# Kernel optimization log

Measured on AMD Instinct MI355X. Metric: run time of the kernel, lower is better.

Reference implementation:

```python
import jax, jax.numpy as jnp
import numpy as np

T, B, I, H, O = 1024, 256, 256, 256, 256


def setup_inputs() -> dict:
    key = jax.random.key(0)
    ks = jax.random.split(key, 12)
    s = 0.01  # init scale matching np.random.normal(0, 0.01)
    return {
        "x_steps": jax.random.normal(ks[0], (T, B, I), dtype=jnp.float32),
        "h": jnp.zeros((B, H), dtype=jnp.float32),
        "w_xr": s * jax.random.normal(ks[1], (I, H), dtype=jnp.float32),
        "w_hr": s * jax.random.normal(ks[2], (H, H), dtype=jnp.float32),
        "b_r": jnp.zeros((H,), dtype=jnp.float32),
        "w_xz": s * jax.random.normal(ks[3], (I, H), dtype=jnp.float32),
        "w_hz": s * jax.random.normal(ks[4], (H, H), dtype=jnp.float32),
        "b_z": jnp.zeros((H,), dtype=jnp.float32),
        "w_xh": s * jax.random.normal(ks[5], (I, H), dtype=jnp.float32),
        "w_hh": s * jax.random.normal(ks[6], (H, H), dtype=jnp.float32),
        "b_h": jnp.zeros((H,), dtype=jnp.float32),
        "w_out": s * jax.random.normal(ks[7], (H, O), dtype=jnp.float32),
        "b_out": jnp.zeros((O,), dtype=jnp.float32),
    }


def reference(x_steps, h, w_xr, w_hr, b_r, w_xz, w_hz, b_z,
              w_xh, w_hh, b_h, w_out, b_out):
    # Precompute all input projections in one batched GEMM per gate: [T,B,H]
    xr = jnp.einsum('tbi,ih->tbh', x_steps, w_xr) + b_r
    xz = jnp.einsum('tbi,ih->tbh', x_steps, w_xz) + b_z
    xh = jnp.einsum('tbi,ih->tbh', x_steps, w_xh) + b_h

    def step(h, xs):
        xr_t, xz_t, xh_t = xs
        r = jax.nn.sigmoid(xr_t + h @ w_hr)
        z = jax.nn.sigmoid(xz_t + h @ w_hz)
        cand = jnp.tanh(xh_t + (r * h) @ w_hh)
        h_new = h * z + (1.0 - z) * cand
        # NOTE: original emits matmul(cand, W_out)+b, using the candidate,
        # not the updated hidden state -- replicate faithfully.
        out = cand @ w_out + b_out
        return h_new, out

    h_final, outs = jax.lax.scan(step, h, (xr, xz, xh))  # outs: [T,B,O]
    return outs.reshape(T * B, O), h_final  # torch.cat(result_list, dim=0)
```

## Files before the change

### kernel.cpp

```cpp
#include <hip/hip_runtime.h>


typedef unsigned short u16t;
typedef unsigned int   u32t;
typedef unsigned long long u64t;
typedef short  s16x8 __attribute__((ext_vector_type(8)));
typedef float  f32x4 __attribute__((ext_vector_type(4)));
typedef float  f32v4 __attribute__((ext_vector_type(4)));
typedef u32t   u32x2 __attribute__((ext_vector_type(2)));

#define L2E 1.4426950408889634f
#define NCONS 112

#define BAR_LDS() asm volatile("s_waitcnt lgkmcnt(0)\n\ts_barrier" ::: "memory")
#define PIN(v) asm volatile("" : "+v"(v))

__device__ __forceinline__ float lo_f(u32t u) {
  return __builtin_bit_cast(float, u << 16);
}
__device__ __forceinline__ float hi_f(u32t u) {
  return __builtin_bit_cast(float, u & 0xffff0000u);
}
__device__ __forceinline__ u32t f2bf(float f) {
  u32t u = __builtin_bit_cast(u32t, f);
  return (u + 0x7fffu + ((u >> 16) & 1u)) >> 16;
}
__device__ __forceinline__ u32t cvtpk(float lo, float hi) {
  u32t r;
  asm("v_cvt_pk_bf16_f32 %0, %1, %2" : "=v"(r) : "v"(lo), "v"(hi));
  return r;
}
__device__ __forceinline__ f32x4 MF(s16x8 a, s16x8 b, f32x4 c) {
  return __builtin_amdgcn_mfma_f32_16x16x32_bf16(a, b, c, 0, 0, 0);
}
__device__ __forceinline__ float sigm2(float y) {
  return __builtin_amdgcn_rcpf(1.0f + __builtin_amdgcn_exp2f(-y));
}
__device__ __forceinline__ float tanh2(float y) {
  return fmaf(-2.0f, __builtin_amdgcn_rcpf(__builtin_amdgcn_exp2f(y) + 1.0f), 1.0f);
}

__global__ void pack_w(const float* __restrict__ wxr, const float* __restrict__ wxz,
                       const float* __restrict__ wxh, const float* __restrict__ whr,
                       const float* __restrict__ whz, const float* __restrict__ whh,
                       const float* __restrict__ wout, u16t* __restrict__ dst,
                       int* __restrict__ prog) {
  if (blockIdx.x == 0 && threadIdx.x < 16) prog[threadIdx.x] = 0;
  int e = blockIdx.x * 256 + threadIdx.x;
  int mat = e >> 16, i = e & 65535;
  const float* src = mat == 0 ? wxr : mat == 1 ? wxz : mat == 2 ? wxh
                   : mat == 3 ? whr : mat == 4 ? whz : mat == 5 ? whh : wout;
  float sc = (mat == 2 || mat == 5) ? 2.0f * L2E : (mat == 6 ? 1.0f : L2E);
  int j = i & 7, lane = (i >> 3) & 63, ks = (i >> 9) & 7, nb = i >> 12;
  int k = ks * 32 + (lane >> 4) * 8 + j;
  int n = nb * 16 + (lane & 15);
  dst[e] = (u16t)f2bf(src[k * 256 + n] * sc);
}

__global__ __launch_bounds__(512, 2) void gru_xproj(
    const float* __restrict__ x, const u16t* __restrict__ wpack,
    const float* __restrict__ br, const float* __restrict__ bz,
    const float* __restrict__ bh,
    u16t* __restrict__ xr_p, u16t* __restrict__ xz_p, u16t* __restrict__ xh_p) {
  __shared__ __align__(128) u16t xt[16384];
  const int tid = threadIdx.x, bid = blockIdx.x;
  const int t = bid >> 2, b0 = (bid & 3) * 64;
  const float* xrow = x + ((size_t)t * 256 + b0) * 256;
#pragma unroll
  for (int c = 0; c < 8; ++c) {
    int f4 = c * 512 + tid;
    f32v4 v = ((const f32v4*)xrow)[f4];
    u32t lo = f2bf(v[0]) | (f2bf(v[1]) << 16);
    u32t hi = f2bf(v[2]) | (f2bf(v[3]) << 16);
    int row = f4 >> 6, c8 = (f4 & 63) * 8;
    int off = (row * 512 + c8) ^ ((row & 7) << 4);
    u32x2 vv; vv[0] = lo; vv[1] = hi;
    *(u32x2*)((char*)xt + off) = vv;
  }
  __syncthreads();
  const int lane = tid & 63, w = tid >> 6;
  const int m2 = w & 1, cg = w >> 1;
  const int arow = m2 * 32 + (lane & 15);
  const int abase = arow * 512 + (lane >> 4) * 16;
  const int asw = (lane & 7) << 4;
  const f32x4 Z = {0.f, 0.f, 0.f, 0.f};
  f32x4 acc[2][12];
#pragma unroll
  for (int s = 0; s < 2; ++s)
#pragma unroll
    for (int p = 0; p < 12; ++p) acc[s][p] = Z;
#pragma unroll
  for (int ks = 0; ks < 8; ++ks) {
    s16x8 a0 = *(const s16x8*)((char*)xt + ((abase + ks * 64) ^ asw));
    s16x8 a1 = *(const s16x8*)((char*)xt + ((abase + 16 * 512 + ks * 64) ^ asw));
#pragma unroll
    for (int p = 0; p < 12; ++p) {
      int pj = cg * 12 + p;
      int gate = pj >> 4, nb = pj & 15;
      const s16x8* wb = (const s16x8*)wpack + gate * 8192;
      s16x8 b = wb[(nb * 8 + ks) * 64 + lane];
      acc[0][p] = MF(a0, b, acc[0][p]);
      acc[1][p] = MF(a1, b, acc[1][p]);
    }
  }
#pragma unroll
  for (int p = 0; p < 12; ++p) {
    int pj = cg * 12 + p;
    int gate = pj >> 4, nb = pj & 15;
    const float* bp = gate == 0 ? br : gate == 1 ? bz : bh;
    float bs = (gate == 2) ? 2.0f * L2E : L2E;
    float bv = bp[nb * 16 + (lane & 15)] * bs;
    u16t* op = gate == 0 ? xr_p : gate == 1 ? xz_p : xh_p;
#pragma unroll
    for (int s = 0; s < 2; ++s) {
      int wg = (b0 >> 4) + m2 * 2 + s;
      u32t lo = f2bf(acc[s][p][0] + bv) | (f2bf(acc[s][p][1] + bv) << 16);
      u32t hi = f2bf(acc[s][p][2] + bv) | (f2bf(acc[s][p][3] + bv) << 16);
      size_t off = (gate == 2)
          ? (size_t)t * 16384 + wg * 1024 + nb * 64 + lane
          : (size_t)t * 32768 + wg * 1024 + nb * 64 + lane;
      u32x2 vv; vv[0] = lo; vv[1] = hi;
      ((u32x2*)op)[off] = vv;
    }
  }
}

#define OFFSW(row, colx2) (((row) * 512 + (colx2)) ^ (((row) & 7) << 4))
#define LDA_HB(ks) (*(const s16x8*)((char*)hb + ((aoff + (ks) * 64) ^ asw)))
#define LDA_RH(ks) (*(const s16x8*)((char*)rh + ((aoff + (ks) * 64) ^ asw)))
#define ZLOAD(buf, ks) do { buf[0] = pz[(ks) * 64]; buf[1] = pz[(ks) * 64 + 512]; } while (0)
#define G1_STEP(buf, ks) do { s16x8 a_ = LDA_HB(ks); \
    ar0 = MF(a_, whr_r[0][ks], ar0); ar1 = MF(a_, whr_r[1][ks], ar1); \
    az0 = MF(a_, buf[0], az0);       az1 = MF(a_, buf[1], az1); } while (0)

__global__ __launch_bounds__(512, 2) void gru_fused(
    const float* __restrict__ h0, const u16t* __restrict__ wpack,
    const u16t* __restrict__ xr_p, const u16t* __restrict__ xz_p,
    const u16t* __restrict__ xh_p, u16t* __restrict__ cand_w,
    const u16t* __restrict__ cand_r, float* __restrict__ hout,
    int* __restrict__ prog, const float* __restrict__ bout,
    float* __restrict__ out) {
  __shared__ __align__(128) u16t smem[16384];
  const int tid = threadIdx.x, lane = tid & 63, w = tid >> 6;
  const int bid = blockIdx.x;

  if (bid < 16) {
    u16t* hb = smem;
    u16t* rh = smem + 4096;
    const int wg = bid;
    const int rlo = (lane >> 4) * 4;
    const int cA = w * 32 + (lane & 15);

    float hr_[2][4];
#pragma unroll
    for (int c = 0; c < 2; ++c)
#pragma unroll
      for (int j = 0; j < 4; ++j)
        hr_[c][j] = h0[(size_t)(wg * 16 + rlo + j) * 256 + cA + c * 16];
#pragma unroll
    for (int c = 0; c < 2; ++c)
#pragma unroll
      for (int j = 0; j < 4; ++j)
        *(u16t*)((char*)hb + OFFSW(rlo + j, (cA + c * 16) * 2)) = (u16t)f2bf(hr_[c][j]);
    __syncthreads();

    const s16x8* pz = (const s16x8*)wpack + 4 * 8192 + w * 1024 + lane;
    const int aoff = (lane & 15) * 512 + (lane >> 4) * 16;
    const int asw = (lane & 7) << 4;

    s16x8 whr_r[2][8], whh_r[2][8];
    {
      const s16x8* prw = (const s16x8*)wpack + 3 * 8192;
      const s16x8* phw = (const s16x8*)wpack + 5 * 8192;
#pragma unroll
      for (int c = 0; c < 2; ++c)
#pragma unroll
        for (int ks = 0; ks < 8; ++ks) {
          int fo = ((2 * w + c) * 8 + ks) * 64 + lane;
          whr_r[c][ks] = prw[fo]; PIN(whr_r[c][ks]);
          whh_r[c][ks] = phw[fo]; PIN(whh_r[c][ks]);
        }
    }

    const size_t xoffRZ = (size_t)wg * 1024 + w * 128 + lane;
    const size_t xoffH  = (size_t)wg * 1024 + w * 128 + lane;
    const u32x2* PXR = (const u32x2*)xr_p;
    const u32x2* PXZ = (const u32x2*)xz_p;
    const u32x2* PXH = (const u32x2*)xh_p;
    u32x2* SXH = (u32x2*)cand_w;

    u32x2 vxr0 = PXR[xoffRZ], vxr1 = PXR[xoffRZ + 64];
    u32x2 vxz0 = PXZ[xoffRZ], vxz1 = PXZ[xoffRZ + 64];
    u32x2 vxh0 = PXH[xoffH],  vxh1 = PXH[xoffH + 64];

    s16x8 bA[2], bB[2];
    ZLOAD(bA, 0);
    ZLOAD(bB, 1);

    for (int t = 0; t < 1024; ++t) {
      f32x4 ar0, ar1, az0, az1;
      ar0[0] = lo_f(vxr0[0]); ar0[1] = hi_f(vxr0[0]); ar0[2] = lo_f(vxr0[1]); ar0[3] = hi_f(vxr0[1]);
      ar1[0] = lo_f(vxr1[0]); ar1[1] = hi_f(vxr1[0]); ar1[2] = lo_f(vxr1[1]); ar1[3] = hi_f(vxr1[1]);
      az0[0] = lo_f(vxz0[0]); az0[1] = hi_f(vxz0[0]); az0[2] = lo_f(vxz0[1]); az0[3] = hi_f(vxz0[1]);
      az1[0] = lo_f(vxz1[0]); az1[1] = hi_f(vxz1[0]); az1[2] = lo_f(vxz1[1]); az1[3] = hi_f(vxz1[1]);

      G1_STEP(bA, 0); ZLOAD(bA, 2);
      G1_STEP(bB, 1); ZLOAD(bB, 3);
      G1_STEP(bA, 2); ZLOAD(bA, 4);
      G1_STEP(bB, 3); ZLOAD(bB, 5);
      G1_STEP(bA, 4); ZLOAD(bA, 6);
      G1_STEP(bB, 5); ZLOAD(bB, 7);
      G1_STEP(bA, 6);
      G1_STEP(bB, 7);

      float r_[2][4];
      r_[0][0] = sigm2(ar0[0]); r_[0][1] = sigm2(ar0[1]); r_[0][2] = sigm2(ar0[2]); r_[0][3] = sigm2(ar0[3]);
      r_[1][0] = sigm2(ar1[0]); r_[1][1] = sigm2(ar1[1]); r_[1][2] = sigm2(ar1[2]); r_[1][3] = sigm2(ar1[3]);

#pragma unroll
      for (int c = 0; c < 2; ++c) {
        u32t p01 = cvtpk(r_[c][0] * hr_[c][0], r_[c][1] * hr_[c][1]);
        u32t p23 = cvtpk(r_[c][2] * hr_[c][2], r_[c][3] * hr_[c][3]);
        *(u16t*)((char*)rh + OFFSW(rlo + 0, (cA + c * 16) * 2)) = (u16t)p01;
        *(u16t*)((char*)rh + OFFSW(rlo + 1, (cA + c * 16) * 2)) = (u16t)(p01 >> 16);
        *(u16t*)((char*)rh + OFFSW(rlo + 2, (cA + c * 16) * 2)) = (u16t)p23;
        *(u16t*)((char*)rh + OFFSW(rlo + 3, (cA + c * 16) * 2)) = (u16t)(p23 >> 16);
      }
      BAR_LDS();

      float z_[2][4];
      z_[0][0] = sigm2(az0[0]); z_[0][1] = sigm2(az0[1]); z_[0][2] = sigm2(az0[2]); z_[0][3] = sigm2(az0[3]);
      z_[1][0] = sigm2(az1[0]); z_[1][1] = sigm2(az1[1]); z_[1][2] = sigm2(az1[2]); z_[1][3] = sigm2(az1[3]);

      f32x4 ac0, ac1;
      ac0[0] = lo_f(vxh0[0]); ac0[1] = hi_f(vxh0[0]); ac0[2] = lo_f(vxh0[1]); ac0[3] = hi_f(vxh0[1]);
      ac1[0] = lo_f(vxh1[0]); ac1[1] = hi_f(vxh1[0]); ac1[2] = lo_f(vxh1[1]); ac1[3] = hi_f(vxh1[1]);

      {
        int tn = t < 1023 ? t + 1 : t;
        size_t oRZ = xoffRZ + (size_t)tn * 32768;
        size_t oH  = xoffH + (size_t)tn * 16384;
        vxr0 = PXR[oRZ]; vxr1 = PXR[oRZ + 64];
        vxz0 = PXZ[oRZ]; vxz1 = PXZ[oRZ + 64];
        vxh0 = PXH[oH];  vxh1 = PXH[oH + 64];
      }

#pragma unroll
      for (int ks = 0; ks < 8; ++ks) {
        s16x8 a_ = LDA_RH(ks);
        ac0 = MF(a_, whh_r[0][ks], ac0);
        ac1 = MF(a_, whh_r[1][ks], ac1);
      }

      float cd[2][4];
      cd[0][0] = tanh2(ac0[0]); cd[0][1] = tanh2(ac0[1]); cd[0][2] = tanh2(ac0[2]); cd[0][3] = tanh2(ac0[3]);
      cd[1][0] = tanh2(ac1[0]); cd[1][1] = tanh2(ac1[1]); cd[1][2] = tanh2(ac1[2]); cd[1][3] = tanh2(ac1[3]);

      size_t ocur = xoffH + (size_t)t * 16384;
      u32x2 s0, s1;
      s0[0] = cvtpk(cd[0][0], cd[0][1]); s0[1] = cvtpk(cd[0][2], cd[0][3]);
      s1[0] = cvtpk(cd[1][0], cd[1][1]); s1[1] = cvtpk(cd[1][2], cd[1][3]);
      __hip_atomic_store((u64t*)(SXH + ocur), __builtin_bit_cast(u64t, s0),
                         __ATOMIC_RELAXED, __HIP_MEMORY_SCOPE_AGENT);
      __hip_atomic_store((u64t*)(SXH + ocur + 64), __builtin_bit_cast(u64t, s1),
                         __ATOMIC_RELAXED, __HIP_MEMORY_SCOPE_AGENT);

#pragma unroll
      for (int c = 0; c < 2; ++c) {
#pragma unroll
        for (int j = 0; j < 4; ++j)
          hr_[c][j] = fmaf(z_[c][j], hr_[c][j] - cd[c][j], cd[c][j]);
        u32t p01 = cvtpk(hr_[c][0], hr_[c][1]);
        u32t p23 = cvtpk(hr_[c][2], hr_[c][3]);
        *(u16t*)((char*)hb + OFFSW(rlo + 0, (cA + c * 16) * 2)) = (u16t)p01;
        *(u16t*)((char*)hb + OFFSW(rlo + 1, (cA + c * 16) * 2)) = (u16t)(p01 >> 16);
        *(u16t*)((char*)hb + OFFSW(rlo + 2, (cA + c * 16) * 2)) = (u16t)p23;
        *(u16t*)((char*)hb + OFFSW(rlo + 3, (cA + c * 16) * 2)) = (u16t)(p23 >> 16);
      }

      ZLOAD(bA, 0);
      ZLOAD(bB, 1);
      BAR_LDS();

      if ((t & 15) == 15) {
        __syncthreads();
        if (tid == 0)
          __hip_atomic_store(prog + wg, t + 1, __ATOMIC_RELAXED,
                             __HIP_MEMORY_SCOPE_AGENT);
      }
    }
#pragma unroll
    for (int c = 0; c < 2; ++c)
#pragma unroll
      for (int j = 0; j < 4; ++j)
        hout[(size_t)(wg * 16 + rlo + j) * 256 + cA + c * 16] = hr_[c][j];

  } else {
    u16t* cm = smem;
    const int cid = bid - 16;
    const s16x8* wo = (const s16x8*)wpack + 6 * 8192;
    const int mt = w & 3, nbs = (w >> 2) * 8;
    const int arow = mt * 16 + (lane & 15);
    const int abase = arow * 512 + (lane >> 4) * 16;
    const int asw = (lane & 7) << 4;
    const f32x4 Z = {0.f, 0.f, 0.f, 0.f};
    int lastmn = 0;

    for (int tile = cid; tile < 4096; tile += NCONS) {
      const int t = tile >> 2, q = tile & 3;
      const int need = t + 1;
      if (lastmn < need) {
        if (tid == 0) {
          int mn;
          for (;;) {
            mn = 1 << 30;
#pragma unroll
            for (int s = 0; s < 16; ++s)
              mn = min(mn, __hip_atomic_load(prog + s, __ATOMIC_RELAXED,
                                             __HIP_MEMORY_SCOPE_AGENT));
            if (mn >= need) break;
            __builtin_amdgcn_s_sleep(8);
            __builtin_amdgcn_s_sleep(8);
            __builtin_amdgcn_s_sleep(8);
            __builtin_amdgcn_s_sleep(8);
          }
          *(int*)cm = mn;
        }
        __syncthreads();
        lastmn = *(volatile int*)cm;
        __syncthreads();
      }
      const u32x2* src = (const u32x2*)cand_r + ((size_t)t * 16 + q * 4) * 1024;
#pragma unroll
      for (int it = 0; it < 8; ++it) {
        int i = it * 512 + tid;
        u32x2 v = __builtin_nontemporal_load(src + i);
        int wg_l = i >> 10, nb = (i >> 6) & 15, ls = i & 63;
        int brow = wg_l * 16 + (ls >> 4) * 4;
        int hc2 = (nb * 16 + (ls & 15)) * 2;
        u16t ev[4] = {(u16t)(v[0] & 0xffff), (u16t)(v[0] >> 16),
                      (u16t)(v[1] & 0xffff), (u16t)(v[1] >> 16)};
#pragma unroll
        for (int j = 0; j < 4; ++j)
          *(u16t*)((char*)cm + OFFSW(brow + j, hc2)) = ev[j];
      }
      __syncthreads();
      f32x4 acc[8] = {Z, Z, Z, Z, Z, Z, Z, Z};
#pragma unroll
      for (int ks = 0; ks < 8; ++ks) {
        s16x8 a = *(const s16x8*)((char*)cm + ((abase + ks * 64) ^ asw));
#pragma unroll
        for (int p = 0; p < 8; ++p)
          acc[p] = MF(a, wo[((nbs + p) * 8 + ks) * 64 + lane], acc[p]);
      }
#pragma unroll
      for (int p = 0; p < 8; ++p) {
        int col = (nbs + p) * 16 + (lane & 15);
        float bv = bout[col];
        size_t rb = (size_t)t * 256 + q * 64 + mt * 16 + (lane >> 4) * 4;
#pragma unroll
        for (int j = 0; j < 4; ++j)
          __builtin_nontemporal_store(acc[p][j] + bv, &out[(rb + j) * 256 + col]);
      }
      __syncthreads();
    }
  }
}

extern "C" void kernel_launch(void* const* d_in, const int* in_sizes, int n_in,
                              void* d_out, int out_size, void* d_ws, size_t ws_size,
                              hipStream_t stream) {
  const float* x    = (const float*)d_in[0];
  const float* h0   = (const float*)d_in[1];
  const float* wxr  = (const float*)d_in[2];
  const float* whr  = (const float*)d_in[3];
  const float* br   = (const float*)d_in[4];
  const float* wxz  = (const float*)d_in[5];
  const float* whz  = (const float*)d_in[6];
  const float* bz   = (const float*)d_in[7];
  const float* wxh  = (const float*)d_in[8];
  const float* whh  = (const float*)d_in[9];
  const float* bh   = (const float*)d_in[10];
  const float* wout = (const float*)d_in[11];
  const float* bout = (const float*)d_in[12];

  float* out  = (float*)d_out;
  u16t* wpack = (u16t*)d_ws;
  int*  prog  = (int*)((char*)d_ws + 917504);
  u16t* xh_p  = (u16t*)((char*)d_ws + (1u << 20));
  u16t* xr_p  = (u16t*)d_out;
  u16t* xz_p  = (u16t*)d_out + 65536;
  float* hout = (float*)((char*)d_out + 268435456ull);

  pack_w<<<1792, 256, 0, stream>>>(wxr, wxz, wxh, whr, whz, whh, wout, wpack, prog);
  gru_xproj<<<4096, 512, 0, stream>>>(x, wpack, br, bz, bh, xr_p, xz_p, xh_p);
  gru_fused<<<16 + NCONS, 512, 0, stream>>>(h0, wpack, xr_p, xz_p, xh_p,
                                            xh_p, xh_p, hout, prog, bout, out);
}
```

Measured before the change: 2.441 ms.

## Fuse input projection into persistent kernel, overlapping it with the recurrence

```diff
diff --git a/kernel.cpp b/kernel.cpp
--- a/kernel.cpp
+++ b/kernel.cpp
@@ -39,13 +39,22 @@
 __device__ __forceinline__ float tanh2(float y) {
   return fmaf(-2.0f, __builtin_amdgcn_rcpf(__builtin_amdgcn_exp2f(y) + 1.0f), 1.0f);
 }
+__device__ __forceinline__ void st_agent(u32x2* p, u32x2 v) {
+  __hip_atomic_store((u64t*)p, __builtin_bit_cast(u64t, v),
+                     __ATOMIC_RELAXED, __HIP_MEMORY_SCOPE_AGENT);
+}
+__device__ __forceinline__ u32x2 ld_agent(const u32x2* p) {
+  return __builtin_bit_cast(u32x2,
+      __hip_atomic_load((const u64t*)p, __ATOMIC_RELAXED,
+                        __HIP_MEMORY_SCOPE_AGENT));
+}
 
 __global__ void pack_w(const float* __restrict__ wxr, const float* __restrict__ wxz,
                        const float* __restrict__ wxh, const float* __restrict__ whr,
                        const float* __restrict__ whz, const float* __restrict__ whh,
                        const float* __restrict__ wout, u16t* __restrict__ dst,
                        int* __restrict__ prog) {
-  if (blockIdx.x == 0 && threadIdx.x < 16) prog[threadIdx.x] = 0;
+  if (blockIdx.x == 0 && threadIdx.x < 128) prog[threadIdx.x] = 0;
   int e = blockIdx.x * 256 + threadIdx.x;
   int mat = e >> 16, i = e & 65535;
   const float* src = mat == 0 ? wxr : mat == 1 ? wxz : mat == 2 ? wxh
@@ -57,74 +66,6 @@
   dst[e] = (u16t)f2bf(src[k * 256 + n] * sc);
 }
 
-__global__ __launch_bounds__(512, 2) void gru_xproj(
-    const float* __restrict__ x, const u16t* __restrict__ wpack,
-    const float* __restrict__ br, const float* __restrict__ bz,
-    const float* __restrict__ bh,
-    u16t* __restrict__ xr_p, u16t* __restrict__ xz_p, u16t* __restrict__ xh_p) {
-  __shared__ __align__(128) u16t xt[16384];
-  const int tid = threadIdx.x, bid = blockIdx.x;
-  const int t = bid >> 2, b0 = (bid & 3) * 64;
-  const float* xrow = x + ((size_t)t * 256 + b0) * 256;
-#pragma unroll
-  for (int c = 0; c < 8; ++c) {
-    int f4 = c * 512 + tid;
-    f32v4 v = ((const f32v4*)xrow)[f4];
-    u32t lo = f2bf(v[0]) | (f2bf(v[1]) << 16);
-    u32t hi = f2bf(v[2]) | (f2bf(v[3]) << 16);
-    int row = f4 >> 6, c8 = (f4 & 63) * 8;
-    int off = (row * 512 + c8) ^ ((row & 7) << 4);
-    u32x2 vv; vv[0] = lo; vv[1] = hi;
-    *(u32x2*)((char*)xt + off) = vv;
-  }
-  __syncthreads();
-  const int lane = tid & 63, w = tid >> 6;
-  const int m2 = w & 1, cg = w >> 1;
-  const int arow = m2 * 32 + (lane & 15);
-  const int abase = arow * 512 + (lane >> 4) * 16;
-  const int asw = (lane & 7) << 4;
-  const f32x4 Z = {0.f, 0.f, 0.f, 0.f};
-  f32x4 acc[2][12];
-#pragma unroll
-  for (int s = 0; s < 2; ++s)
-#pragma unroll
-    for (int p = 0; p < 12; ++p) acc[s][p] = Z;
-#pragma unroll
-  for (int ks = 0; ks < 8; ++ks) {
-    s16x8 a0 = *(const s16x8*)((char*)xt + ((abase + ks * 64) ^ asw));
-    s16x8 a1 = *(const s16x8*)((char*)xt + ((abase + 16 * 512 + ks * 64) ^ asw));
-#pragma unroll
-    for (int p = 0; p < 12; ++p) {
-      int pj = cg * 12 + p;
-      int gate = pj >> 4, nb = pj & 15;
-      const s16x8* wb = (const s16x8*)wpack + gate * 8192;
-      s16x8 b = wb[(nb * 8 + ks) * 64 + lane];
-      acc[0][p] = MF(a0, b, acc[0][p]);
-      acc[1][p] = MF(a1, b, acc[1][p]);
-    }
-  }
-#pragma unroll
-  for (int p = 0; p < 12; ++p) {
-    int pj = cg * 12 + p;
-    int gate = pj >> 4, nb = pj & 15;
-    const float* bp = gate == 0 ? br : gate == 1 ? bz : bh;
-    float bs = (gate == 2) ? 2.0f * L2E : L2E;
-    float bv = bp[nb * 16 + (lane & 15)] * bs;
-    u16t* op = gate == 0 ? xr_p : gate == 1 ? xz_p : xh_p;
-#pragma unroll
-    for (int s = 0; s < 2; ++s) {
-      int wg = (b0 >> 4) + m2 * 2 + s;
-      u32t lo = f2bf(acc[s][p][0] + bv) | (f2bf(acc[s][p][1] + bv) << 16);
-      u32t hi = f2bf(acc[s][p][2] + bv) | (f2bf(acc[s][p][3] + bv) << 16);
-      size_t off = (gate == 2)
-          ? (size_t)t * 16384 + wg * 1024 + nb * 64 + lane
-          : (size_t)t * 32768 + wg * 1024 + nb * 64 + lane;
-      u32x2 vv; vv[0] = lo; vv[1] = hi;
-      ((u32x2*)op)[off] = vv;
-    }
-  }
-}
-
 #define OFFSW(row, colx2) (((row) * 512 + (colx2)) ^ (((row) & 7) << 4))
 #define LDA_HB(ks) (*(const s16x8*)((char*)hb + ((aoff + (ks) * 64) ^ asw)))
 #define LDA_RH(ks) (*(const s16x8*)((char*)rh + ((aoff + (ks) * 64) ^ asw)))
@@ -134,15 +75,18 @@
     az0 = MF(a_, buf[0], az0);       az1 = MF(a_, buf[1], az1); } while (0)
 
 __global__ __launch_bounds__(512, 2) void gru_fused(
-    const float* __restrict__ h0, const u16t* __restrict__ wpack,
-    const u16t* __restrict__ xr_p, const u16t* __restrict__ xz_p,
-    const u16t* __restrict__ xh_p, u16t* __restrict__ cand_w,
-    const u16t* __restrict__ cand_r, float* __restrict__ hout,
-    int* __restrict__ prog, const float* __restrict__ bout,
-    float* __restrict__ out) {
+    const float* __restrict__ x, const float* __restrict__ h0,
+    const u16t* __restrict__ wpack,
+    const float* __restrict__ br, const float* __restrict__ bz,
+    const float* __restrict__ bh,
+    u16t* __restrict__ xr_p, u16t* __restrict__ xz_p, u16t* __restrict__ xh_p,
+    float* __restrict__ hout, int* __restrict__ prog,
+    const float* __restrict__ bout, float* __restrict__ out) {
   __shared__ __align__(128) u16t smem[16384];
+  __shared__ __align__(16) int bc[4];
   const int tid = threadIdx.x, lane = tid & 63, w = tid >> 6;
   const int bid = blockIdx.x;
+  int* xprog = prog + 16;
 
   if (bid < 16) {
     u16t* hb = smem;
@@ -187,7 +131,29 @@
     const u32x2* PXR = (const u32x2*)xr_p;
     const u32x2* PXZ = (const u32x2*)xz_p;
     const u32x2* PXH = (const u32x2*)xh_p;
-    u32x2* SXH = (u32x2*)cand_w;
+    u32x2* SXH = (u32x2*)xh_p;
+
+    int Mcur = 0;
+    {
+      const int Mreq = 8 * 17 + 8;
+      if (tid == 0) {
+        int M;
+        for (;;) {
+          M = 1 << 30;
+#pragma unroll 16
+          for (int c2 = 0; c2 < NCONS; ++c2)
+            M = min(M, __hip_atomic_load(xprog + c2, __ATOMIC_RELAXED,
+                                         __HIP_MEMORY_SCOPE_AGENT));
+          if (M >= Mreq) break;
+          __builtin_amdgcn_s_sleep(8);
+          __builtin_amdgcn_s_sleep(8);
+        }
+        bc[0] = M;
+      }
+      __syncthreads();
+      Mcur = bc[0];
+      __syncthreads();
+    }
 
     u32x2 vxr0 = PXR[xoffRZ], vxr1 = PXR[xoffRZ + 64];
     u32x2 vxz0 = PXZ[xoffRZ], vxz1 = PXZ[xoffRZ + 64];
@@ -198,6 +164,30 @@
     ZLOAD(bB, 1);
 
     for (int t = 0; t < 1024; ++t) {
+      if ((t & 15) == 0 && t > 0) {
+        int treq = t + 17; if (treq > 1023) treq = 1023;
+        int Mreq = 8 * treq + 8;
+        if (Mcur < Mreq) {
+          if (tid == 0) {
+            int M;
+            for (;;) {
+              M = 1 << 30;
+#pragma unroll 16
+              for (int c2 = 0; c2 < NCONS; ++c2)
+                M = min(M, __hip_atomic_load(xprog + c2, __ATOMIC_RELAXED,
+                                             __HIP_MEMORY_SCOPE_AGENT));
+              if (M >= Mreq) break;
+              __builtin_amdgcn_s_sleep(8);
+              __builtin_amdgcn_s_sleep(8);
+            }
+            bc[0] = M;
+          }
+          __syncthreads();
+          Mcur = bc[0];
+          __syncthreads();
+        }
+      }
+
       f32x4 ar0, ar1, az0, az1;
       ar0[0] = lo_f(vxr0[0]); ar0[1] = hi_f(vxr0[0]); ar0[2] = lo_f(vxr0[1]); ar0[3] = hi_f(vxr0[1]);
       ar1[0] = lo_f(vxr1[0]); ar1[1] = hi_f(vxr1[0]); ar1[2] = lo_f(vxr1[1]); ar1[3] = hi_f(vxr1[1]);
@@ -260,10 +250,8 @@
       u32x2 s0, s1;
       s0[0] = cvtpk(cd[0][0], cd[0][1]); s0[1] = cvtpk(cd[0][2], cd[0][3]);
       s1[0] = cvtpk(cd[1][0], cd[1][1]); s1[1] = cvtpk(cd[1][2], cd[1][3]);
-      __hip_atomic_store((u64t*)(SXH + ocur), __builtin_bit_cast(u64t, s0),
-                         __ATOMIC_RELAXED, __HIP_MEMORY_SCOPE_AGENT);
-      __hip_atomic_store((u64t*)(SXH + ocur + 64), __builtin_bit_cast(u64t, s1),
-                         __ATOMIC_RELAXED, __HIP_MEMORY_SCOPE_AGENT);
+      st_agent(SXH + ocur, s0);
+      st_agent(SXH + ocur + 64, s1);
 
 #pragma unroll
       for (int c = 0; c < 2; ++c) {
@@ -298,11 +286,75 @@
   } else {
     u16t* cm = smem;
     const int cid = bid - 16;
+    const int asw = (lane & 7) << 4;
+
+    for (int i = cid; i < 8192; i += NCONS) {
+      const int t = i >> 3, q = (i >> 1) & 3, hh = i & 1;
+      const float* xrow = x + ((size_t)t * 256 + q * 64) * 256;
+#pragma unroll
+      for (int c = 0; c < 8; ++c) {
+        int f4 = c * 512 + tid;
+        f32v4 v = ((const f32v4*)xrow)[f4];
+        u32t lo = f2bf(v[0]) | (f2bf(v[1]) << 16);
+        u32t hi = f2bf(v[2]) | (f2bf(v[3]) << 16);
+        int row = f4 >> 6, c8 = (f4 & 63) * 8;
+        int off = (row * 512 + c8) ^ ((row & 7) << 4);
+        u32x2 vv; vv[0] = lo; vv[1] = hi;
+        *(u32x2*)((char*)cm + off) = vv;
+      }
+      __syncthreads();
+      const int m2 = w & 1, cg = w >> 1;
+      const int arow = m2 * 32 + (lane & 15);
+      const int abase = arow * 512 + (lane >> 4) * 16;
+      const f32x4 Z = {0.f, 0.f, 0.f, 0.f};
+      f32x4 acc[2][6];
+#pragma unroll
+      for (int s = 0; s < 2; ++s)
+#pragma unroll
+        for (int p = 0; p < 6; ++p) acc[s][p] = Z;
+#pragma unroll
+      for (int ks = 0; ks < 8; ++ks) {
+        s16x8 a0 = *(const s16x8*)((char*)cm + ((abase + ks * 64) ^ asw));
+        s16x8 a1 = *(const s16x8*)((char*)cm + ((abase + 16 * 512 + ks * 64) ^ asw));
+#pragma unroll
+        for (int p = 0; p < 6; ++p) {
+          int pj = hh * 24 + cg * 6 + p;
+          int gate = pj >> 4, nb = pj & 15;
+          s16x8 b = ((const s16x8*)wpack + gate * 8192)[(nb * 8 + ks) * 64 + lane];
+          acc[0][p] = MF(a0, b, acc[0][p]);
+          acc[1][p] = MF(a1, b, acc[1][p]);
+        }
+      }
+#pragma unroll
+      for (int p = 0; p < 6; ++p) {
+        int pj = hh * 24 + cg * 6 + p;
+        int gate = pj >> 4, nb = pj & 15;
+        const float* bp = gate == 0 ? br : gate == 1 ? bz : bh;
+        float bs = (gate == 2) ? 2.0f * L2E : L2E;
+        float bv = bp[nb * 16 + (lane & 15)] * bs;
+        u16t* op = gate == 0 ? xr_p : gate == 1 ? xz_p : xh_p;
+#pragma unroll
+        for (int s = 0; s < 2; ++s) {
+          int wg2 = q * 4 + m2 * 2 + s;
+          u32t lo = f2bf(acc[s][p][0] + bv) | (f2bf(acc[s][p][1] + bv) << 16);
+          u32t hi = f2bf(acc[s][p][2] + bv) | (f2bf(acc[s][p][3] + bv) << 16);
+          size_t off = (gate == 2)
+              ? (size_t)t * 16384 + wg2 * 1024 + nb * 64 + lane
+              : (size_t)t * 32768 + wg2 * 1024 + nb * 64 + lane;
+          u32x2 vv; vv[0] = lo; vv[1] = hi;
+          st_agent((u32x2*)op + off, vv);
+        }
+      }
+      __syncthreads();
+      if (tid == 0)
+        __hip_atomic_store(xprog + cid, i + NCONS, __ATOMIC_RELAXED,
+                           __HIP_MEMORY_SCOPE_AGENT);
+    }
+
     const s16x8* wo = (const s16x8*)wpack + 6 * 8192;
     const int mt = w & 3, nbs = (w >> 2) * 8;
     const int arow = mt * 16 + (lane & 15);
     const int abase = arow * 512 + (lane >> 4) * 16;
-    const int asw = (lane & 7) << 4;
     const f32x4 Z = {0.f, 0.f, 0.f, 0.f};
     int lastmn = 0;
 
@@ -324,17 +376,17 @@
             __builtin_amdgcn_s_sleep(8);
             __builtin_amdgcn_s_sleep(8);
           }
-          *(int*)cm = mn;
+          bc[0] = mn;
         }
         __syncthreads();
-        lastmn = *(volatile int*)cm;
+        lastmn = bc[0];
         __syncthreads();
       }
-      const u32x2* src = (const u32x2*)cand_r + ((size_t)t * 16 + q * 4) * 1024;
+      const u32x2* src = (const u32x2*)xh_p + ((size_t)t * 16 + q * 4) * 1024;
 #pragma unroll
       for (int it = 0; it < 8; ++it) {
         int i = it * 512 + tid;
-        u32x2 v = __builtin_nontemporal_load(src + i);
+        u32x2 v = ld_agent(src + i);
         int wg_l = i >> 10, nb = (i >> 6) & 15, ls = i & 63;
         int brow = wg_l * 16 + (ls >> 4) * 4;
         int hc2 = (nb * 16 + (ls & 15)) * 2;
@@ -393,7 +445,7 @@
   float* hout = (float*)((char*)d_out + 268435456ull);
 
   pack_w<<<1792, 256, 0, stream>>>(wxr, wxz, wxh, whr, whz, whh, wout, wpack, prog);
-  gru_xproj<<<4096, 512, 0, stream>>>(x, wpack, br, bz, bh, xr_p, xz_p, xh_p);
-  gru_fused<<<16 + NCONS, 512, 0, stream>>>(h0, wpack, xr_p, xz_p, xh_p,
-                                            xh_p, xh_p, hout, prog, bout, out);
-}
+  gru_fused<<<16 + NCONS, 512, 0, stream>>>(x, h0, wpack, br, bz, bh,
+                                            xr_p, xz_p, xh_p, hout, prog,
+                                            bout, out);
+}
```

Result: faster. 2.216 ms (-9.3%).
